# Performance work log

Measured on AMD Instinct MI355X. Metric: run time of the kernel, lower is better.

Reference implementation:

```python
import jax, jax.numpy as jnp
import numpy as np
import math

B, S, D, H, M, R = 4, 1024, 1024, 16, 4, 64
DH = D // H
EPS = 1e-8

def setup_inputs() -> dict:
    key = jax.random.key(0)
    ks = jax.random.split(key, 8)
    sc = 0.02
    return {
        'x': jax.random.normal(ks[0], (B, S, D), jnp.float32),
        'Wk': jax.random.normal(ks[1], (D, D), jnp.float32) * sc,
        'bk': jnp.zeros((D,), jnp.float32),
        'Wq': jax.random.normal(ks[2], (D, D), jnp.float32) * sc,
        'bq': jnp.zeros((D,), jnp.float32),
        'Wv': jax.random.normal(ks[3], (D, D), jnp.float32) * sc,
        'bv': jnp.zeros((D,), jnp.float32),
        'mask1': jax.random.normal(ks[4], (M, R, S), jnp.float32) * sc,
        'mask2': jax.random.normal(ks[5], (M, R, S), jnp.float32) * sc,
        'roll_back': jax.random.randint(ks[6], (M, S, S), 0, S, jnp.int64),
    }

def reference(x, Wk, bk, Wq, bq, Wv, bv, mask1, mask2, roll_back):
    def proj(W, b):
        # torch Linear: x @ W^T + b ; reshape to [B, H, S, DH]
        y = jnp.dot(x, W.T) + b
        return y.reshape(B, S, H, DH).transpose(0, 2, 1, 3)
    k = proj(Wk, bk)
    q = proj(Wq, bq)
    v = proj(Wv, bv)
    # learnable low-rank mask: [M, S, S]
    learnable_mask = jnp.einsum('mrs,mrt->mst', mask1, mask2)
    # gather along last dim with roll_back indices
    gathered = jnp.take_along_axis(learnable_mask, roll_back, axis=-1)  # [M, S, S]
    att = jnp.einsum('bhsd,bhtd->bhst', q, k) / math.sqrt(DH)  # [B, H, S, S]
    att = att.reshape(B, H // M, M, S, S) * gathered[None, None]
    att = att.reshape(B, H, S, S)
    # Frobenius norm over last two dims per (B, H)
    fro = jnp.sqrt(jnp.sum(att * att, axis=(-2, -1), keepdims=True))
    att = att / (fro + EPS)
    out = jnp.einsum('bhst,bhtd->bhsd', att, v)
    return out.transpose(0, 2, 1, 3).reshape(B, S, D)
```

## Files before the change

kernel.cpp:

```cpp
#include <hip/hip_runtime.h>
#include <hip/hip_bf16.h>
#include <stdint.h>

typedef __attribute__((ext_vector_type(8))) __bf16 bf16x8;
typedef __attribute__((ext_vector_type(4))) float  f32x4;
typedef __attribute__((ext_vector_type(16))) float f32x16;

__device__ __forceinline__ ushort f2bf(float f) {
    union { float f; uint32_t u; } v; v.f = f;
    uint32_t u = v.u;
    uint32_t r = 0x7FFFu + ((u >> 16) & 1u);
    return (ushort)((u + r) >> 16);
}
__device__ __forceinline__ float bf2f(ushort u) {
    union { uint32_t u; float f; } v; v.u = ((uint32_t)u) << 16;
    return v.f;
}

typedef __attribute__((address_space(3))) uint32_t lds_u32_t;
typedef const __attribute__((address_space(1))) uint32_t glb_u32_t;
__device__ __forceinline__ void async_copy16(const void* g, void* l) {
    __builtin_amdgcn_global_load_lds((glb_u32_t*)g, (lds_u32_t*)l, 16, 0, 0);
}

__global__ __launch_bounds__(256) void convert_all(
    const float* __restrict__ x, const float* __restrict__ wk,
    const float* __restrict__ wq, const float* __restrict__ wv,
    ushort* __restrict__ xb, ushort* __restrict__ wball)
{
    int i = blockIdx.x * 256 + threadIdx.x;
    const float* src; ushort* dst; int j;
    if (i < 1048576) { src = x; dst = xb; j = i; }
    else {
        int t = i - 1048576;
        int z = t >> 18;
        j = t & 262143;
        src = (z == 0) ? wk : (z == 1) ? wq : wv;
        dst = wball + z * 1048576;
    }
    float4 f = ((const float4*)src)[j];
    ushort4 o;
    o.x = f2bf(f.x); o.y = f2bf(f.y); o.z = f2bf(f.z); o.w = f2bf(f.w);
    ((ushort4*)dst)[j] = o;
}

__global__ __launch_bounds__(256) void proj_gemm(
    const ushort* __restrict__ xb, const ushort* __restrict__ wball,
    const float* __restrict__ bk, const float* __restrict__ bq, const float* __restrict__ bv,
    ushort* __restrict__ kd, ushort* __restrict__ qd, ushort* __restrict__ vd)
{
    __shared__ ushort As[3 * 128 * 32];
    __shared__ ushort Bs[3 * 128 * 32];
    const int z = blockIdx.z;
    const int row0 = blockIdx.x * 128;
    const int col0 = blockIdx.y * 128;
    const ushort* wb = wball + z * 1048576;
    const int tid = threadIdx.x;
    const int lane = tid & 63, wave = tid >> 6;
    const int quad = lane >> 4, m15 = lane & 15;
    const int wr = wave >> 1, wc = wave & 1;

    f32x4 acc[4][4];
    for (int i = 0; i < 4; i++)
        for (int j = 0; j < 4; j++) acc[i][j] = (f32x4){0.f, 0.f, 0.f, 0.f};

#define STAGE(BI, KK) do {                                                        \
        _Pragma("unroll")                                                         \
        for (int i_ = 0; i_ < 2; i_++) {                                          \
            int c_ = tid + i_ * 256;                                  \
            int r_ = c_ >> 2, cjp_ = c_ & 3;                                      \
            int cj_ = cjp_ ^ ((r_ >> 1) & 3);                                     \
            async_copy16(&xb[(row0 + r_) * 1024 + (KK) + cj_ * 8],                \
                         &As[(BI) * 4096 + c_ * 8]);                              \
            async_copy16(&wb[(col0 + r_) * 1024 + (KK) + cj_ * 8],                \
                         &Bs[(BI) * 4096 + c_ * 8]);                              \
        }                                                                         \
    } while (0)

#define COMPUTE(BI) do {                                                          \
        const ushort* a_ = &As[(BI) * 4096];                                      \
        const ushort* b_ = &Bs[(BI) * 4096];                                      \
        bf16x8 af[4], bfv[4];                                                     \
        _Pragma("unroll")                                                         \
        for (int fr = 0; fr < 4; fr++) {                                          \
            int row = wr * 64 + fr * 16 + m15;                                    \
            af[fr] = *(const bf16x8*)&a_[row * 32 + ((quad ^ ((row >> 1) & 3)) * 8)]; \
        }                                                                         \
        _Pragma("unroll")                                                         \
        for (int fc = 0; fc < 4; fc++) {                                          \
            int row = wc * 64 + fc * 16 + m15;                                    \
            bfv[fc] = *(const bf16x8*)&b_[row * 32 + ((quad ^ ((row >> 1) & 3)) * 8)]; \
        }                                                                         \
        _Pragma("unroll")                                                         \
        for (int fr = 0; fr < 4; fr++)                                            \
            _Pragma("unroll")                                                     \
            for (int fc = 0; fc < 4; fc++)                                        \
                acc[fr][fc] = __builtin_amdgcn_mfma_f32_16x16x32_bf16(            \
                    af[fr], bfv[fc], acc[fr][fc], 0, 0, 0);                       \
    } while (0)

    STAGE(0, 0);
    STAGE(1, 32);

    int cur = 0;
    #pragma unroll 3
    for (int t = 0; t < 30; ++t) {
        int sb = cur + 2; if (sb >= 3) sb -= 3;
        STAGE(sb, (t + 2) * 32);
        asm volatile("s_waitcnt vmcnt(8)" ::: "memory");
        __builtin_amdgcn_s_barrier();
        COMPUTE(cur);
        __builtin_amdgcn_s_barrier();
        cur = (cur == 2) ? 0 : cur + 1;
    }
    asm volatile("s_waitcnt vmcnt(4)" ::: "memory");
    __builtin_amdgcn_s_barrier();
    COMPUTE(cur);
    cur = (cur == 2) ? 0 : cur + 1;
    asm volatile("s_waitcnt vmcnt(0)" ::: "memory");
    __builtin_amdgcn_s_barrier();
    COMPUTE(cur);

#undef STAGE
#undef COMPUTE

    const float* bias = (z == 0) ? bk : (z == 1) ? bq : bv;
    ushort* dstA = (z == 0) ? kd : qd;
    for (int fr = 0; fr < 4; fr++) {
        int ibase = row0 + wr * 64 + fr * 16 + quad * 4;
        int b_ = ibase >> 10, s = ibase & 1023;
        for (int fc = 0; fc < 4; fc++) {
            int j = col0 + wc * 64 + fc * 16 + m15;
            int h = j >> 6, dh = j & 63;
            float bb = bias[j];
            if (z < 2) {
                for (int r = 0; r < 4; r++)
                    dstA[((b_ * 16 + h) * 1024 + (s + r)) * 64 + dh] = f2bf(acc[fr][fc][r] + bb);
            } else {
                ushort4 o;
                o.x = f2bf(acc[fr][fc][0] + bb);
                o.y = f2bf(acc[fr][fc][1] + bb);
                o.z = f2bf(acc[fr][fc][2] + bb);
                o.w = f2bf(acc[fr][fc][3] + bb);
                *(ushort4*)&vd[((b_ * 16 + h) * 64 + dh) * 1024 + s] = o;
            }
        }
    }
}

__global__ __launch_bounds__(256) void mask_fused(
    const float* __restrict__ m1, const float* __restrict__ m2,
    const int* __restrict__ rb, ushort* __restrict__ gth)
{
    __shared__ float As8[64 * 8];
    __shared__ float lmS[8 * 1024];
    const int s0 = blockIdx.x * 8;
    const int m = blockIdx.y;
    const int tid = threadIdx.x;

    if (tid < 128) {
        int r = tid >> 1, half = tid & 1;
        *(float4*)&As8[r * 8 + half * 4] =
            *(const float4*)&m1[(m * 64 + r) * 1024 + s0 + half * 4];
    }
    __syncthreads();

    f32x4 acc8[8];
    #pragma unroll
    for (int s = 0; s < 8; s++) acc8[s] = (f32x4){0.f, 0.f, 0.f, 0.f};
    const float* m2b = m2 + m * 65536 + tid * 4;
    #pragma unroll 4
    for (int r = 0; r < 64; r++) {
        float4 b4 = *(const float4*)&m2b[r * 1024];
        f32x4 b = (f32x4){b4.x, b4.y, b4.z, b4.w};
        #pragma unroll
        for (int s = 0; s < 8; s++) {
            float a = As8[r * 8 + s];
            acc8[s] += a * b;
        }
    }
    #pragma unroll
    for (int s = 0; s < 8; s++)
        *(f32x4*)&lmS[s * 1024 + tid * 4] = acc8[s];
    __syncthreads();

    const int base = (m * 1024 + s0) * 1024;
    #pragma unroll
    for (int i = 0; i < 8; i++) {
        int c = tid + i * 256;
        int row = c >> 8, j = (c & 255) * 4;
        int4 idx = *(const int4*)&rb[base + row * 1024 + j];
        ushort4 o;
        o.x = f2bf(lmS[row * 1024 + (idx.x & 1023)] * 0.125f);
        o.y = f2bf(lmS[row * 1024 + (idx.y & 1023)] * 0.125f);
        o.z = f2bf(lmS[row * 1024 + (idx.z & 1023)] * 0.125f);
        o.w = f2bf(lmS[row * 1024 + (idx.w & 1023)] * 0.125f);
        *(ushort4*)&gth[base + row * 1024 + j] = o;
    }
}

__global__ __launch_bounds__(256, 4) void attention(
    const ushort* __restrict__ qd, const ushort* __restrict__ kd, const ushort* __restrict__ vd,
    const ushort* __restrict__ gth, float* __restrict__ O, float* __restrict__ ss)
{
    __shared__ ushort Ks[64 * 72];
    __shared__ ushort Vs[64 * 72];
    __shared__ ushort Ps[64 * 72];
    __shared__ ushort Ms[64 * 76];
    __shared__ float red[4];
    const int s0 = blockIdx.x * 64;
    const int bh = blockIdx.y;
    const int mm = bh & 3;
    const int tid = threadIdx.x, lane = tid & 63, wave = tid >> 6;
    const int l31 = lane & 31, hl = lane >> 5;
    const int wr2 = wave >> 1, wc2 = wave & 1;

    const int r0_ = tid >> 3,          o0_ = (tid & 7) * 8;
    const int r1_ = (tid + 256) >> 3,  o1_ = ((tid + 256) & 7) * 8;

    const ushort* kdb = kd + bh * 65536;
    const ushort* vdb = vd + bh * 65536;
    const ushort* gbase = gth + mm * 1048576 + s0 * 1024;

    const int srow = wr2 * 32 + l31;
    const int tb   = wc2 * 32 + 4 * hl;
    const int f_   = (srow >> 3) & 1;

    *(uint4*)&Ks[r0_ * 72 + o0_] = *(const uint4*)&qd[(bh * 1024 + s0 + r0_) * 64 + o0_];
    *(uint4*)&Ks[r1_ * 72 + o1_] = *(const uint4*)&qd[(bh * 1024 + s0 + r1_) * 64 + o1_];
    uint4 kr0 = *(const uint4*)&kdb[r0_ * 64 + o0_];
    uint4 kr1 = *(const uint4*)&kdb[r1_ * 64 + o1_];
    uint4 vr0 = *(const uint4*)&vdb[r0_ * 1024 + o0_];
    uint4 vr1 = *(const uint4*)&vdb[r1_ * 1024 + o1_];
    uint4 mr0 = *(const uint4*)&gbase[r0_ * 1024 + o0_];
    uint4 mr1 = *(const uint4*)&gbase[r1_ * 1024 + o1_];
    __syncthreads();
    bf16x8 qf[4];
    #pragma unroll
    for (int kk = 0; kk < 4; kk++)
        qf[kk] = *(const bf16x8*)&Ks[srow * 72 + kk * 16 + hl * 8];
    __syncthreads();

    *(uint4*)&Ks[r0_ * 72 + o0_] = kr0;
    *(uint4*)&Ks[r1_ * 72 + o1_] = kr1;
    *(uint4*)&Vs[r0_ * 72 + o0_] = vr0;
    *(uint4*)&Vs[r1_ * 72 + o1_] = vr1;
    *(uint2*)&Ms[r0_ * 76 + o0_]     = make_uint2(mr0.x, mr0.y);
    *(uint2*)&Ms[r0_ * 76 + o0_ + 4] = make_uint2(mr0.z, mr0.w);
    *(uint2*)&Ms[r1_ * 76 + o1_]     = make_uint2(mr1.x, mr1.y);
    *(uint2*)&Ms[r1_ * 76 + o1_ + 4] = make_uint2(mr1.z, mr1.w);
    kr0 = *(const uint4*)&kdb[(64 + r0_) * 64 + o0_];
    kr1 = *(const uint4*)&kdb[(64 + r1_) * 64 + o1_];
    vr0 = *(const uint4*)&vdb[r0_ * 1024 + 64 + o0_];
    vr1 = *(const uint4*)&vdb[r1_ * 1024 + 64 + o1_];
    mr0 = *(const uint4*)&gbase[r0_ * 1024 + 64 + o0_];
    mr1 = *(const uint4*)&gbase[r1_ * 1024 + 64 + o1_];
    __syncthreads();

    f32x16 oacc;
    #pragma unroll
    for (int i = 0; i < 16; i++) oacc[i] = 0.f;
    float ss0 = 0.f, ss1 = 0.f, ss2 = 0.f, ss3 = 0.f;

    for (int t = 0; t < 16; ++t) {
        f32x16 p;
        #pragma unroll
        for (int i = 0; i < 16; i++) p[i] = 0.f;
        #pragma unroll
        for (int kk = 0; kk < 4; kk++) {
            bf16x8 kf = *(const bf16x8*)&Ks[(wc2 * 32 + l31) * 72 + kk * 16 + hl * 8];
            p = __builtin_amdgcn_mfma_f32_32x32x16_bf16(kf, qf[kk], p, 0, 0, 0);
        }
        #pragma unroll
        for (int g = 0; g < 4; g++) {
            ushort4 mk = *(const ushort4*)&Ms[srow * 76 + tb + 8 * g];
            float pv0 = p[4 * g + 0] * bf2f(mk.x);
            float pv1 = p[4 * g + 1] * bf2f(mk.y);
            float pv2 = p[4 * g + 2] * bf2f(mk.z);
            float pv3 = p[4 * g + 3] * bf2f(mk.w);
            ss0 += pv0 * pv0; ss1 += pv1 * pv1;
            ss2 += pv2 * pv2; ss3 += pv3 * pv3;
            ushort4 o_;
            o_.x = f2bf(pv0); o_.y = f2bf(pv1);
            o_.z = f2bf(pv2); o_.w = f2bf(pv3);
            int u_ = (wc2 * 8 + hl + 2 * g) ^ f_;
            *(ushort4*)&Ps[srow * 72 + u_ * 4] = o_;
        }
        __syncthreads();
        #pragma unroll
        for (int kk = 0; kk < 4; kk++) {
            int m2 = kk * 4 + hl * 2;
            union { uint2 u2[2]; bf16x8 v; } av;
            av.u2[0] = *(const uint2*)&Ps[srow * 72 + ((m2 ^ f_) * 4)];
            av.u2[1] = *(const uint2*)&Ps[srow * 72 + (((m2 + 1) ^ f_) * 4)];
            bf16x8 b = *(const bf16x8*)&Vs[(wc2 * 32 + l31) * 72 + kk * 16 + hl * 8];
            oacc = __builtin_amdgcn_mfma_f32_32x32x16_bf16(av.v, b, oacc, 0, 0, 0);
        }
        __syncthreads();
        if (t < 15) {
            *(uint4*)&Ks[r0_ * 72 + o0_] = kr0;
            *(uint4*)&Ks[r1_ * 72 + o1_] = kr1;
            *(uint4*)&Vs[r0_ * 72 + o0_] = vr0;
            *(uint4*)&Vs[r1_ * 72 + o1_] = vr1;
            *(uint2*)&Ms[r0_ * 76 + o0_]     = make_uint2(mr0.x, mr0.y);
            *(uint2*)&Ms[r0_ * 76 + o0_ + 4] = make_uint2(mr0.z, mr0.w);
            *(uint2*)&Ms[r1_ * 76 + o1_]     = make_uint2(mr1.x, mr1.y);
            *(uint2*)&Ms[r1_ * 76 + o1_ + 4] = make_uint2(mr1.z, mr1.w);
            if (t < 14) {
                const int tn = (t + 2) * 64;
                kr0 = *(const uint4*)&kdb[(tn + r0_) * 64 + o0_];
                kr1 = *(const uint4*)&kdb[(tn + r1_) * 64 + o1_];
                vr0 = *(const uint4*)&vdb[r0_ * 1024 + tn + o0_];
                vr1 = *(const uint4*)&vdb[r1_ * 1024 + tn + o1_];
                mr0 = *(const uint4*)&gbase[r0_ * 1024 + tn + o0_];
                mr1 = *(const uint4*)&gbase[r1_ * 1024 + tn + o1_];
            }
            __syncthreads();
        }
    }
    #pragma unroll
    for (int reg = 0; reg < 16; reg++) {
        int s = s0 + wr2 * 32 + (reg & 3) + 8 * (reg >> 2) + 4 * hl;
        int dh = wc2 * 32 + l31;
        O[(bh * 1024 + s) * 64 + dh] = oacc[reg];
    }
    float ssacc = (ss0 + ss1) + (ss2 + ss3);
    for (int off = 32; off; off >>= 1) ssacc += __shfl_down(ssacc, off, 64);
    if (lane == 0) red[wave] = ssacc;
    __syncthreads();
    if (tid == 0) atomicAdd(&ss[bh], red[0] + red[1] + red[2] + red[3]);
}

__global__ __launch_bounds__(256) void normalize_out(const float* __restrict__ O,
                                                     const float* __restrict__ ss,
                                                     float* __restrict__ out)
{
    int gid = blockIdx.x * 256 + threadIdx.x;
    int e = gid * 4;
    int bh = e >> 16;
    float inv = 1.f / (sqrtf(ss[bh]) + 1e-8f);
    float4 v4 = *(const float4*)&O[e];
    int b_ = bh >> 4, h = bh & 15;
    int s = (e >> 6) & 1023, dh = e & 63;
    float4 o4 = {v4.x * inv, v4.y * inv, v4.z * inv, v4.w * inv};
    *(float4*)&out[((b_ * 1024 + s) * 16 + h) * 64 + dh] = o4;
}

extern "C" void kernel_launch(void* const* d_in, const int* in_sizes, int n_in,
                              void* d_out, int out_size, void* d_ws, size_t ws_size,
                              hipStream_t stream) {
    const float* x  = (const float*)d_in[0];
    const float* Wk = (const float*)d_in[1];
    const float* bk = (const float*)d_in[2];
    const float* Wq = (const float*)d_in[3];
    const float* bq = (const float*)d_in[4];
    const float* Wv = (const float*)d_in[5];
    const float* bv = (const float*)d_in[6];
    const float* m1 = (const float*)d_in[7];
    const float* m2 = (const float*)d_in[8];
    const int*   rb = (const int*)d_in[9];
    float* out = (float*)d_out;

    char* ws = (char*)d_ws;
    ushort* xb    = (ushort*)(ws);
    ushort* wball = (ushort*)(ws + 8388608);
    ushort* kd    = (ushort*)(ws + 14680064);
    ushort* qd    = (ushort*)(ws + 23068672);
    ushort* vd    = (ushort*)(ws + 31457280);
    float*  O     = (float*)(ws + 39845888);
    ushort* gth   = (ushort*)(ws + 56623104);
    float*  ssb   = (float*)(ws + 65011712);

    convert_all<<<7168, 256, 0, stream>>>(x, Wk, Wq, Wv, xb, wball);
    proj_gemm<<<dim3(32, 8, 3), 256, 0, stream>>>(xb, wball, bk, bq, bv, kd, qd, vd);
    mask_fused<<<dim3(128, 4), 256, 0, stream>>>(m1, m2, rb, gth);
    hipMemsetAsync(ssb, 0, 64 * sizeof(float), stream);
    attention<<<dim3(16, 64), 256, 0, stream>>>(qd, kd, vd, gth, O, ssb);
    normalize_out<<<4096, 256, 0, stream>>>(O, ssb, out);
}
```

Measured before the change: 193.0 us.

## Keep P in registers via permlane32 swap and split PV across key halves

Removes the LDS round-trip for the masked score tile P. Each wave repacks its own P fragment into the MFMA A-operand layout with permlane32_swap. It then computes a partial PV over its own 32-key slice for both dh halves, and the two column-waves' partial outputs are summed through LDS at the end. This removes the Ps buffer and one barrier per tile, and adds s_setprio hints around the MFMA bursts. In exchange there are twice as many accumulator registers, which may hurt occupancy under launch_bounds(256,4), plus an epilogue reduction.

```diff
diff --git a/kernel.cpp b/kernel.cpp
--- a/kernel.cpp
+++ b/kernel.cpp
@@ -15,6 +15,9 @@
 __device__ __forceinline__ float bf2f(ushort u) {
     union { uint32_t u; float f; } v; v.u = ((uint32_t)u) << 16;
     return v.f;
+}
+__device__ __forceinline__ unsigned packbf(float lo, float hi) {
+    return (unsigned)f2bf(lo) | ((unsigned)f2bf(hi) << 16);
 }
 
 typedef __attribute__((address_space(3))) uint32_t lds_u32_t;
@@ -203,11 +206,13 @@
     const ushort* __restrict__ qd, const ushort* __restrict__ kd, const ushort* __restrict__ vd,
     const ushort* __restrict__ gth, float* __restrict__ O, float* __restrict__ ss)
 {
-    __shared__ ushort Ks[64 * 72];
-    __shared__ ushort Vs[64 * 72];
-    __shared__ ushort Ps[64 * 72];
-    __shared__ ushort Ms[64 * 76];
-    __shared__ float red[4];
+    __shared__ __align__(16) char ldsraw[28176];
+    ushort* Ks  = (ushort*)ldsraw;
+    ushort* Vs  = (ushort*)(ldsraw + 9216);
+    ushort* Ms  = (ushort*)(ldsraw + 18432);
+    float*  red = (float*)(ldsraw + 28160);
+    float*  fbuf = (float*)ldsraw;
+
     const int s0 = blockIdx.x * 64;
     const int bh = blockIdx.y;
     const int mm = bh & 3;
@@ -224,7 +229,6 @@
 
     const int srow = wr2 * 32 + l31;
     const int tb   = wc2 * 32 + 4 * hl;
-    const int f_   = (srow >> 3) & 1;
 
     *(uint4*)&Ks[r0_ * 72 + o0_] = *(const uint4*)&qd[(bh * 1024 + s0 + r0_) * 64 + o0_];
     *(uint4*)&Ks[r1_ * 72 + o1_] = *(const uint4*)&qd[(bh * 1024 + s0 + r1_) * 64 + o1_];
@@ -257,20 +261,23 @@
     mr1 = *(const uint4*)&gbase[r1_ * 1024 + 64 + o1_];
     __syncthreads();
 
-    f32x16 oacc;
+    f32x16 oaccA, oaccB;
     #pragma unroll
-    for (int i = 0; i < 16; i++) oacc[i] = 0.f;
+    for (int i = 0; i < 16; i++) { oaccA[i] = 0.f; oaccB[i] = 0.f; }
     float ss0 = 0.f, ss1 = 0.f, ss2 = 0.f, ss3 = 0.f;
 
     for (int t = 0; t < 16; ++t) {
         f32x16 p;
         #pragma unroll
         for (int i = 0; i < 16; i++) p[i] = 0.f;
+        __builtin_amdgcn_s_setprio(1);
         #pragma unroll
         for (int kk = 0; kk < 4; kk++) {
             bf16x8 kf = *(const bf16x8*)&Ks[(wc2 * 32 + l31) * 72 + kk * 16 + hl * 8];
             p = __builtin_amdgcn_mfma_f32_32x32x16_bf16(kf, qf[kk], p, 0, 0, 0);
         }
+        __builtin_amdgcn_s_setprio(0);
+        unsigned u[8];
         #pragma unroll
         for (int g = 0; g < 4; g++) {
             ushort4 mk = *(const ushort4*)&Ms[srow * 76 + tb + 8 * g];
@@ -280,22 +287,30 @@
             float pv3 = p[4 * g + 3] * bf2f(mk.w);
             ss0 += pv0 * pv0; ss1 += pv1 * pv1;
             ss2 += pv2 * pv2; ss3 += pv3 * pv3;
-            ushort4 o_;
-            o_.x = f2bf(pv0); o_.y = f2bf(pv1);
-            o_.z = f2bf(pv2); o_.w = f2bf(pv3);
-            int u_ = (wc2 * 8 + hl + 2 * g) ^ f_;
-            *(ushort4*)&Ps[srow * 72 + u_ * 4] = o_;
-        }
-        __syncthreads();
-        #pragma unroll
-        for (int kk = 0; kk < 4; kk++) {
-            int m2 = kk * 4 + hl * 2;
-            union { uint2 u2[2]; bf16x8 v; } av;
-            av.u2[0] = *(const uint2*)&Ps[srow * 72 + ((m2 ^ f_) * 4)];
-            av.u2[1] = *(const uint2*)&Ps[srow * 72 + (((m2 + 1) ^ f_) * 4)];
-            bf16x8 b = *(const bf16x8*)&Vs[(wc2 * 32 + l31) * 72 + kk * 16 + hl * 8];
-            oacc = __builtin_amdgcn_mfma_f32_32x32x16_bf16(av.v, b, oacc, 0, 0, 0);
-        }
+            u[2 * g]     = packbf(pv0, pv1);
+            u[2 * g + 1] = packbf(pv2, pv3);
+        }
+        auto r02 = __builtin_amdgcn_permlane32_swap(u[0], u[2], false, false);
+        auto r13 = __builtin_amdgcn_permlane32_swap(u[1], u[3], false, false);
+        auto r46 = __builtin_amdgcn_permlane32_swap(u[4], u[6], false, false);
+        auto r57 = __builtin_amdgcn_permlane32_swap(u[5], u[7], false, false);
+        union { unsigned q[4]; bf16x8 v; } af0, af1;
+        af0.q[0] = r02[0]; af0.q[1] = r13[0]; af0.q[2] = r02[1]; af0.q[3] = r13[1];
+        af1.q[0] = r46[0]; af1.q[1] = r57[0]; af1.q[2] = r46[1]; af1.q[3] = r57[1];
+        __builtin_amdgcn_s_setprio(1);
+        {
+            const ushort* vrA = &Vs[l31 * 72 + wc2 * 32];
+            bf16x8 b00 = *(const bf16x8*)&vrA[hl * 8];
+            bf16x8 b01 = *(const bf16x8*)&vrA[16 + hl * 8];
+            oaccA = __builtin_amdgcn_mfma_f32_32x32x16_bf16(af0.v, b00, oaccA, 0, 0, 0);
+            oaccA = __builtin_amdgcn_mfma_f32_32x32x16_bf16(af1.v, b01, oaccA, 0, 0, 0);
+            const ushort* vrB = &Vs[(32 + l31) * 72 + wc2 * 32];
+            bf16x8 b10 = *(const bf16x8*)&vrB[hl * 8];
+            bf16x8 b11 = *(const bf16x8*)&vrB[16 + hl * 8];
+            oaccB = __builtin_amdgcn_mfma_f32_32x32x16_bf16(af0.v, b10, oaccB, 0, 0, 0);
+            oaccB = __builtin_amdgcn_mfma_f32_32x32x16_bf16(af1.v, b11, oaccB, 0, 0, 0);
+        }
+        __builtin_amdgcn_s_setprio(0);
         __syncthreads();
         if (t < 15) {
             *(uint4*)&Ks[r0_ * 72 + o0_] = kr0;
@@ -318,11 +333,26 @@
             __syncthreads();
         }
     }
-    #pragma unroll
-    for (int reg = 0; reg < 16; reg++) {
-        int s = s0 + wr2 * 32 + (reg & 3) + 8 * (reg >> 2) + 4 * hl;
-        int dh = wc2 * 32 + l31;
-        O[(bh * 1024 + s) * 64 + dh] = oacc[reg];
+
+    if (wc2 == 1) {
+        #pragma unroll
+        for (int reg = 0; reg < 16; reg++) {
+            int row = wr2 * 32 + (reg & 3) + 8 * (reg >> 2) + 4 * hl;
+            fbuf[row * 66 + l31]      = oaccA[reg];
+            fbuf[row * 66 + 32 + l31] = oaccB[reg];
+        }
+    }
+    __syncthreads();
+    if (wc2 == 0) {
+        #pragma unroll
+        for (int reg = 0; reg < 16; reg++) {
+            int rl = (reg & 3) + 8 * (reg >> 2) + 4 * hl;
+            int s = s0 + wr2 * 32 + rl;
+            float a = oaccA[reg] + fbuf[(wr2 * 32 + rl) * 66 + l31];
+            float b = oaccB[reg] + fbuf[(wr2 * 32 + rl) * 66 + 32 + l31];
+            O[(bh * 1024 + s) * 64 + l31]      = a;
+            O[(bh * 1024 + s) * 64 + 32 + l31] = b;
+        }
     }
     float ssacc = (ss0 + ss1) + (ss2 + ss3);
     for (int off = 32; off; off >>= 1) ssacc += __shfl_down(ssacc, off, 64);
```

After: 186.8 us. -3.2%, faster.
